# Optimization experiments

Hardware: AMD Instinct MI355X
Metric: run time of the kernel (lower is better)

The kernel has to match this reference:

```python
import jax, jax.numpy as jnp
import numpy as np

TOKENS = 8192
HIDDEN = 4096
EPS = 1e-6
FP8_MAX = 448.0  # max finite value of float8_e4m3fn


def setup_inputs() -> dict:
    key = jax.random.key(0)
    k1, k2, k3 = jax.random.split(key, 3)
    x = jax.random.normal(k1, (TOKENS, HIDDEN), jnp.float32)
    # RMSNorm gains near 1
    norm_w = 1.0 + 0.1 * jax.random.normal(k2, (4, HIDDEN), jnp.float32)
    Ws = 0.02 * jax.random.normal(k3, (3, HIDDEN, HIDDEN), jnp.float32)
    # static per-tensor weight scales (amax / fp8_max)
    w_scales = jnp.max(jnp.abs(Ws), axis=(1, 2)) / FP8_MAX
    return {"x": x, "norm_w": norm_w, "Ws": Ws, "w_scales": w_scales}


def _rmsnorm(x, w):
    var = jnp.mean(x * x, axis=-1, keepdims=True)
    return x * jax.lax.rsqrt(var + EPS) * w


def _quant_dequant_fp8(v, s):
    # quantize to e4m3 with scale s, then dequantize (emulated fp8 GEMM inputs)
    q = (v / s).astype(jnp.float8_e4m3fn)
    return q.astype(jnp.float32) * s


def _fp8_linear(y, W, w_scale):
    # dynamic per-token activation scale
    a_scale = jnp.maximum(jnp.max(jnp.abs(y), axis=-1, keepdims=True) / FP8_MAX, 1e-12)
    yq = _quant_dequant_fp8(y, a_scale)           # [T, H]
    Wq = _quant_dequant_fp8(W, w_scale)           # [H, H]
    return yq @ Wq.T                              # torch.nn.Linear convention


def reference(x, norm_w, Ws, w_scales):
    x = jax.nn.relu(x)
    resid = x
    y = _rmsnorm(x, norm_w[0])                    # plain RMSNorm
    for i in range(3):
        h = _fp8_linear(y, Ws[i], w_scales[i])    # FP8 GEMM
        resid = h + resid                         # fused add + RMSNorm
        y = _rmsnorm(resid, norm_w[i + 1])
    return y
```

## Files before the change

kernel.cpp:

```cpp
#include <hip/hip_runtime.h>
#include <stdint.h>

#define TOKENS 8192
#define HIDDEN 4096
constexpr float EPS = 1e-6f;
constexpr float FP8_MAX = 448.0f;

using f32x4  = __attribute__((ext_vector_type(4))) float;
using f32x16 = __attribute__((ext_vector_type(16))) float;
using i32x4  = __attribute__((ext_vector_type(4))) int;
using i32x8  = __attribute__((ext_vector_type(8))) int;

typedef __attribute__((address_space(3))) uint32_t lds_u32_t;
typedef const __attribute__((address_space(1))) uint32_t glb_u32_t;

__device__ inline uint32_t pack_fp8x4(float a, float b, float c, float d) {
    int w = 0;
    w = __builtin_amdgcn_cvt_pk_fp8_f32(a, b, w, false);
    w = __builtin_amdgcn_cvt_pk_fp8_f32(c, d, w, true);
    return (uint32_t)w;
}

__device__ inline float block_sum(float v, float* sh, int tid) {
#pragma unroll
    for (int o = 32; o > 0; o >>= 1) v += __shfl_xor(v, o, 64);
    if ((tid & 63) == 0) sh[tid >> 6] = v;
    __syncthreads();
    return sh[0] + sh[1] + sh[2] + sh[3];
}
__device__ inline float block_max(float v, float* sh, int tid) {
#pragma unroll
    for (int o = 32; o > 0; o >>= 1) v = fmaxf(v, __shfl_xor(v, o, 64));
    if ((tid & 63) == 0) sh[tid >> 6] = v;
    __syncthreads();
    return fmaxf(fmaxf(sh[0], sh[1]), fmaxf(sh[2], sh[3]));
}

__launch_bounds__(256)
__global__ void quant_weights(const float* __restrict__ Ws,
                              const float* __restrict__ w_scales,
                              uint8_t* __restrict__ Wq) {
    size_t idx = ((size_t)blockIdx.x * 256 + threadIdx.x) * 8;
    int tensor = (int)(idx / ((size_t)HIDDEN * HIDDEN));
    float inv = 1.0f / w_scales[tensor];
    const float4* src = (const float4*)(Ws + idx);
    float4 v0 = src[0], v1 = src[1];
    uint2 out;
    out.x = pack_fp8x4(v0.x * inv, v0.y * inv, v0.z * inv, v0.w * inv);
    out.y = pack_fp8x4(v1.x * inv, v1.y * inv, v1.z * inv, v1.w * inv);
    *(uint2*)(Wq + idx) = out;
}

__launch_bounds__(256)
__global__ void relu_rms_quant(const float* __restrict__ x,
                               const float* __restrict__ nw,
                               float* __restrict__ resid,
                               uint8_t* __restrict__ yq,
                               float* __restrict__ ascale) {
    __shared__ float sh1[4], sh2[4];
    const int row = blockIdx.x, tid = threadIdx.x;
    const float* xr = x + (size_t)row * HIDDEN;
    float* rr = resid + (size_t)row * HIDDEN;

    float4 v[4];
    float ss = 0.f;
#pragma unroll
    for (int c = 0; c < 4; ++c) {
        float4 t = *(const float4*)(xr + c * 1024 + tid * 4);
        t.x = fmaxf(t.x, 0.f); t.y = fmaxf(t.y, 0.f);
        t.z = fmaxf(t.z, 0.f); t.w = fmaxf(t.w, 0.f);
        v[c] = t;
        ss += t.x * t.x + t.y * t.y + t.z * t.z + t.w * t.w;
        *(float4*)(rr + c * 1024 + tid * 4) = t;
    }
    ss = block_sum(ss, sh1, tid);
    float rstd = 1.0f / sqrtf(ss * (1.0f / HIDDEN) + EPS);

    float4 y[4];
    float amax = 0.f;
#pragma unroll
    for (int c = 0; c < 4; ++c) {
        float4 w = *(const float4*)(nw + c * 1024 + tid * 4);
        y[c].x = v[c].x * rstd * w.x; amax = fmaxf(amax, fabsf(y[c].x));
        y[c].y = v[c].y * rstd * w.y; amax = fmaxf(amax, fabsf(y[c].y));
        y[c].z = v[c].z * rstd * w.z; amax = fmaxf(amax, fabsf(y[c].z));
        y[c].w = v[c].w * rstd * w.w; amax = fmaxf(amax, fabsf(y[c].w));
    }
    amax = block_max(amax, sh2, tid);
    float s = fmaxf(amax / FP8_MAX, 1e-12f);
    if (tid == 0) ascale[row] = s;
    float inv = 1.0f / s;
#pragma unroll
    for (int c = 0; c < 4; ++c) {
        uint32_t p = pack_fp8x4(y[c].x * inv, y[c].y * inv, y[c].z * inv, y[c].w * inv);
        *(uint32_t*)(yq + (size_t)row * HIDDEN + c * 1024 + tid * 4) = p;
    }
}

__launch_bounds__(256)
__global__ void rms_quant(const float* __restrict__ resid,
                          const float* __restrict__ nw,
                          uint8_t* __restrict__ yq,
                          float* __restrict__ ascale) {
    __shared__ float sh1[4], sh2[4];
    const int row = blockIdx.x, tid = threadIdx.x;
    const float* rr = resid + (size_t)row * HIDDEN;

    float4 v[4];
    float ss = 0.f;
#pragma unroll
    for (int c = 0; c < 4; ++c) {
        float4 t = *(const float4*)(rr + c * 1024 + tid * 4);
        v[c] = t;
        ss += t.x * t.x + t.y * t.y + t.z * t.z + t.w * t.w;
    }
    ss = block_sum(ss, sh1, tid);
    float rstd = 1.0f / sqrtf(ss * (1.0f / HIDDEN) + EPS);

    float4 y[4];
    float amax = 0.f;
#pragma unroll
    for (int c = 0; c < 4; ++c) {
        float4 w = *(const float4*)(nw + c * 1024 + tid * 4);
        y[c].x = v[c].x * rstd * w.x; amax = fmaxf(amax, fabsf(y[c].x));
        y[c].y = v[c].y * rstd * w.y; amax = fmaxf(amax, fabsf(y[c].y));
        y[c].z = v[c].z * rstd * w.z; amax = fmaxf(amax, fabsf(y[c].z));
        y[c].w = v[c].w * rstd * w.w; amax = fmaxf(amax, fabsf(y[c].w));
    }
    amax = block_max(amax, sh2, tid);
    float s = fmaxf(amax / FP8_MAX, 1e-12f);
    if (tid == 0) ascale[row] = s;
    float inv = 1.0f / s;
#pragma unroll
    for (int c = 0; c < 4; ++c) {
        uint32_t p = pack_fp8x4(y[c].x * inv, y[c].y * inv, y[c].z * inv, y[c].w * inv);
        *(uint32_t*)(yq + (size_t)row * HIDDEN + c * 1024 + tid * 4) = p;
    }
}

__launch_bounds__(256)
__global__ void rms_final(const float* __restrict__ resid,
                          const float* __restrict__ nw,
                          float* __restrict__ out) {
    __shared__ float sh1[4];
    const int row = blockIdx.x, tid = threadIdx.x;
    const float* rr = resid + (size_t)row * HIDDEN;

    float4 v[4];
    float ss = 0.f;
#pragma unroll
    for (int c = 0; c < 4; ++c) {
        float4 t = *(const float4*)(rr + c * 1024 + tid * 4);
        v[c] = t;
        ss += t.x * t.x + t.y * t.y + t.z * t.z + t.w * t.w;
    }
    ss = block_sum(ss, sh1, tid);
    float rstd = 1.0f / sqrtf(ss * (1.0f / HIDDEN) + EPS);

#pragma unroll
    for (int c = 0; c < 4; ++c) {
        float4 w = *(const float4*)(nw + c * 1024 + tid * 4);
        float4 o;
        o.x = v[c].x * rstd * w.x;
        o.y = v[c].y * rstd * w.y;
        o.z = v[c].z * rstd * w.z;
        o.w = v[c].w * rstd * w.w;
        *(float4*)(out + (size_t)row * HIDDEN + c * 1024 + tid * 4) = o;
    }
}

#define BM 128
#define BN 128
#define BK 64

__launch_bounds__(256)
__global__ void gemm_fp8(const uint8_t* __restrict__ Aq,
                         const uint8_t* __restrict__ Bq,
                         const float* __restrict__ ascale,
                         const float* __restrict__ wscale_p,
                         float* __restrict__ resid) {
    __shared__ __align__(16) uint8_t sA[2][BM * BK];
    __shared__ __align__(16) uint8_t sB[2][BN * BK];
    __shared__ float s_as[BM];

    const int tid = threadIdx.x;
    int bid = blockIdx.x;
    bid = (bid & 7) * 256 + (bid >> 3);
    const int nbn = HIDDEN / BN;
    const int bm = bid / nbn, bn = bid % nbn;
    const int brow = bm * BM, bcol = bn * BN;

    const int wave = tid >> 6, lane = tid & 63;
    const int wm = wave >> 1, wn = wave & 1;
    const int lr = lane & 31;
    const int lh = lane >> 5;

    if (tid < BM) s_as[tid] = ascale[brow + tid];

    f32x16 acc[2][2] = {};

    const uint8_t* aSrc = Aq + (size_t)brow * HIDDEN;
    const uint8_t* bSrc = Bq + (size_t)bcol * HIDDEN;

    const int r_st = tid >> 2;
    const int g_st = tid & 3;
    const int gsrc = g_st ^ ((r_st >> 1) & 3);
    const size_t off0 = (size_t)r_st * HIDDEN + gsrc * 16;
    const size_t off1 = (size_t)(r_st + 64) * HIDDEN + gsrc * 16;
    const int lds0 = wave * 1024;
    const int lds1 = 4096 + wave * 1024;

    int offA[2][2], offB[2][2];
#pragma unroll
    for (int m = 0; m < 2; ++m) {
        int ra = wm * 64 + m * 32 + lr;
        int sa_ = (ra >> 1) & 3;
        offA[m][0] = ra * 64 + ((2 * lh + 0) ^ sa_) * 16;
        offA[m][1] = ra * 64 + ((2 * lh + 1) ^ sa_) * 16;
        int rb = wn * 64 + m * 32 + lr;
        int sb_ = (rb >> 1) & 3;
        offB[m][0] = rb * 64 + ((2 * lh + 0) ^ sb_) * 16;
        offB[m][1] = rb * 64 + ((2 * lh + 1) ^ sb_) * 16;
    }

    const int UNIT = 0x7F7F7F7F;

    auto stage = [&](int buf, int k0) {
        __builtin_amdgcn_global_load_lds((glb_u32_t*)(aSrc + off0 + k0),
                                         (lds_u32_t*)&sA[buf][lds0], 16, 0, 0);
        __builtin_amdgcn_global_load_lds((glb_u32_t*)(aSrc + off1 + k0),
                                         (lds_u32_t*)&sA[buf][lds1], 16, 0, 0);
        __builtin_amdgcn_global_load_lds((glb_u32_t*)(bSrc + off0 + k0),
                                         (lds_u32_t*)&sB[buf][lds0], 16, 0, 0);
        __builtin_amdgcn_global_load_lds((glb_u32_t*)(bSrc + off1 + k0),
                                         (lds_u32_t*)&sB[buf][lds1], 16, 0, 0);
    };
    auto compute = [&](int buf) {
        i32x8 a[2], b[2];
#pragma unroll
        for (int m = 0; m < 2; ++m) {
            i32x4 lo = *(const i32x4*)&sA[buf][offA[m][0]];
            i32x4 hi = *(const i32x4*)&sA[buf][offA[m][1]];
            a[m] = __builtin_shufflevector(lo, hi, 0, 1, 2, 3, 4, 5, 6, 7);
        }
#pragma unroll
        for (int n = 0; n < 2; ++n) {
            i32x4 lo = *(const i32x4*)&sB[buf][offB[n][0]];
            i32x4 hi = *(const i32x4*)&sB[buf][offB[n][1]];
            b[n] = __builtin_shufflevector(lo, hi, 0, 1, 2, 3, 4, 5, 6, 7);
        }
#pragma unroll
        for (int m = 0; m < 2; ++m)
#pragma unroll
            for (int n = 0; n < 2; ++n)
                acc[m][n] = __builtin_amdgcn_mfma_scale_f32_32x32x64_f8f6f4(
                    a[m], b[n], acc[m][n], 0, 0, 0, UNIT, 0, UNIT);
    };

    stage(0, 0);
    __syncthreads();

    const int NT = HIDDEN / BK;
    for (int t = 0; t < NT; t += 2) {
        stage(1, (t + 1) * BK);
        compute(0);
        __syncthreads();
        if (t + 2 < NT) stage(0, (t + 2) * BK);
        compute(1);
        __syncthreads();
    }

    const float wsc = *wscale_p;
#pragma unroll
    for (int m = 0; m < 2; ++m)
#pragma unroll
        for (int n = 0; n < 2; ++n) {
            const int col = bcol + wn * 64 + n * 32 + lr;
#pragma unroll
            for (int i = 0; i < 16; ++i) {
                const int rl = (i & 3) + 8 * (i >> 2) + 4 * lh;
                const int row_local = wm * 64 + m * 32 + rl;
                const float alpha = s_as[row_local] * wsc;
                const size_t o = (size_t)(brow + row_local) * HIDDEN + col;
                resid[o] += acc[m][n][i] * alpha;
            }
        }
}

extern "C" void kernel_launch(void* const* d_in, const int* in_sizes, int n_in,
                              void* d_out, int out_size, void* d_ws, size_t ws_size,
                              hipStream_t stream) {
    const float* x   = (const float*)d_in[0];
    const float* nw  = (const float*)d_in[1];
    const float* Ws  = (const float*)d_in[2];
    const float* wsc = (const float*)d_in[3];
    float* out = (float*)d_out;

    uint8_t* ws = (uint8_t*)d_ws;
    float*   resid  = (float*)ws;
    uint8_t* yq     = ws + (size_t)TOKENS * HIDDEN * 4;
    uint8_t* Wq     = yq + (size_t)TOKENS * HIDDEN;
    float*   ascale = (float*)(Wq + (size_t)3 * HIDDEN * HIDDEN);

    quant_weights<<<(3 * (size_t)HIDDEN * HIDDEN) / 2048, 256, 0, stream>>>(Ws, wsc, Wq);

    relu_rms_quant<<<TOKENS, 256, 0, stream>>>(x, nw, resid, yq, ascale);

    for (int i = 0; i < 3; ++i) {
        gemm_fp8<<<(TOKENS / BM) * (HIDDEN / BN), 256, 0, stream>>>(
            yq, Wq + (size_t)i * HIDDEN * HIDDEN, ascale, wsc + i, resid);
        if (i < 2)
            rms_quant<<<TOKENS, 256, 0, stream>>>(resid, nw + (size_t)(i + 1) * HIDDEN, yq, ascale);
        else
            rms_final<<<TOKENS, 256, 0, stream>>>(resid, nw + (size_t)3 * HIDDEN, out);
    }
}
```

Measured before the change: 788.6 us.

## Enlarge FP8 GEMM tile to 256x256 with 4-stage LDS pipeline

The GEMM tile grows from 128x128 to 256x256 with 512 threads (8 waves, each owning a 128x64 sub-tile). Double buffering with two full barriers per k-step becomes a 4-buffer ring that prefetches two stages ahead, using explicit vmcnt waits and one barrier per step. MFMA issue is wrapped in s_setprio, and the per-row activation-scale load is moved after the main loop. The aim is more operand reuse per byte of global traffic and better hiding of load latency. The cost is 128 KB of LDS per block and higher register pressure, which may limit occupancy.

Result: faster. 691.0 us (-12.4%).

```diff
diff --git a/kernel.cpp b/kernel.cpp
--- a/kernel.cpp
+++ b/kernel.cpp
@@ -169,35 +169,34 @@
     }
 }
 
-#define BM 128
-#define BN 128
+#define BM 256
+#define BN 256
 #define BK 64
-
-__launch_bounds__(256)
+#define NBUF 4
+
+__launch_bounds__(512, 2)
 __global__ void gemm_fp8(const uint8_t* __restrict__ Aq,
                          const uint8_t* __restrict__ Bq,
                          const float* __restrict__ ascale,
                          const float* __restrict__ wscale_p,
                          float* __restrict__ resid) {
-    __shared__ __align__(16) uint8_t sA[2][BM * BK];
-    __shared__ __align__(16) uint8_t sB[2][BN * BK];
+    __shared__ __align__(16) uint8_t sA[NBUF][BM * BK];
+    __shared__ __align__(16) uint8_t sB[NBUF][BN * BK];
     __shared__ float s_as[BM];
 
     const int tid = threadIdx.x;
     int bid = blockIdx.x;
-    bid = (bid & 7) * 256 + (bid >> 3);
+    bid = (bid & 7) * 64 + (bid >> 3);
     const int nbn = HIDDEN / BN;
     const int bm = bid / nbn, bn = bid % nbn;
     const int brow = bm * BM, bcol = bn * BN;
 
     const int wave = tid >> 6, lane = tid & 63;
-    const int wm = wave >> 1, wn = wave & 1;
+    const int wm = wave >> 2, wn = wave & 3;
     const int lr = lane & 31;
     const int lh = lane >> 5;
 
-    if (tid < BM) s_as[tid] = ascale[brow + tid];
-
-    f32x16 acc[2][2] = {};
+    f32x16 acc[4][2] = {};
 
     const uint8_t* aSrc = Aq + (size_t)brow * HIDDEN;
     const uint8_t* bSrc = Bq + (size_t)bcol * HIDDEN;
@@ -206,83 +205,94 @@
     const int g_st = tid & 3;
     const int gsrc = g_st ^ ((r_st >> 1) & 3);
     const size_t off0 = (size_t)r_st * HIDDEN + gsrc * 16;
-    const size_t off1 = (size_t)(r_st + 64) * HIDDEN + gsrc * 16;
-    const int lds0 = wave * 1024;
-    const int lds1 = 4096 + wave * 1024;
-
-    int offA[2][2], offB[2][2];
-#pragma unroll
-    for (int m = 0; m < 2; ++m) {
-        int ra = wm * 64 + m * 32 + lr;
-        int sa_ = (ra >> 1) & 3;
-        offA[m][0] = ra * 64 + ((2 * lh + 0) ^ sa_) * 16;
-        offA[m][1] = ra * 64 + ((2 * lh + 1) ^ sa_) * 16;
-        int rb = wn * 64 + m * 32 + lr;
-        int sb_ = (rb >> 1) & 3;
-        offB[m][0] = rb * 64 + ((2 * lh + 0) ^ sb_) * 16;
-        offB[m][1] = rb * 64 + ((2 * lh + 1) ^ sb_) * 16;
+    const size_t off1 = (size_t)(r_st + 128) * HIDDEN + gsrc * 16;
+    const int ldsw = wave * 1024;
+
+    int offA[4][2], offB[2][2];
+#pragma unroll
+    for (int mi = 0; mi < 4; ++mi) {
+        int ra = wm * 128 + mi * 32 + lr;
+        int sw = (ra >> 1) & 3;
+        offA[mi][0] = ra * 64 + ((2 * lh + 0) ^ sw) * 16;
+        offA[mi][1] = ra * 64 + ((2 * lh + 1) ^ sw) * 16;
+    }
+#pragma unroll
+    for (int ni = 0; ni < 2; ++ni) {
+        int rb = wn * 64 + ni * 32 + lr;
+        int sw = (rb >> 1) & 3;
+        offB[ni][0] = rb * 64 + ((2 * lh + 0) ^ sw) * 16;
+        offB[ni][1] = rb * 64 + ((2 * lh + 1) ^ sw) * 16;
     }
 
     const int UNIT = 0x7F7F7F7F;
 
-    auto stage = [&](int buf, int k0) {
+    auto stage = [&](int buf, int kt) {
+        const int k0 = kt * BK;
         __builtin_amdgcn_global_load_lds((glb_u32_t*)(aSrc + off0 + k0),
-                                         (lds_u32_t*)&sA[buf][lds0], 16, 0, 0);
+                                         (lds_u32_t*)&sA[buf][ldsw], 16, 0, 0);
         __builtin_amdgcn_global_load_lds((glb_u32_t*)(aSrc + off1 + k0),
-                                         (lds_u32_t*)&sA[buf][lds1], 16, 0, 0);
+                                         (lds_u32_t*)&sA[buf][8192 + ldsw], 16, 0, 0);
         __builtin_amdgcn_global_load_lds((glb_u32_t*)(bSrc + off0 + k0),
-                                         (lds_u32_t*)&sB[buf][lds0], 16, 0, 0);
+                                         (lds_u32_t*)&sB[buf][ldsw], 16, 0, 0);
         __builtin_amdgcn_global_load_lds((glb_u32_t*)(bSrc + off1 + k0),
-                                         (lds_u32_t*)&sB[buf][lds1], 16, 0, 0);
+                                         (lds_u32_t*)&sB[buf][8192 + ldsw], 16, 0, 0);
     };
     auto compute = [&](int buf) {
-        i32x8 a[2], b[2];
-#pragma unroll
-        for (int m = 0; m < 2; ++m) {
-            i32x4 lo = *(const i32x4*)&sA[buf][offA[m][0]];
-            i32x4 hi = *(const i32x4*)&sA[buf][offA[m][1]];
-            a[m] = __builtin_shufflevector(lo, hi, 0, 1, 2, 3, 4, 5, 6, 7);
+        i32x8 a[4], b[2];
+#pragma unroll
+        for (int mi = 0; mi < 4; ++mi) {
+            i32x4 lo = *(const i32x4*)&sA[buf][offA[mi][0]];
+            i32x4 hi = *(const i32x4*)&sA[buf][offA[mi][1]];
+            a[mi] = __builtin_shufflevector(lo, hi, 0, 1, 2, 3, 4, 5, 6, 7);
         }
 #pragma unroll
-        for (int n = 0; n < 2; ++n) {
-            i32x4 lo = *(const i32x4*)&sB[buf][offB[n][0]];
-            i32x4 hi = *(const i32x4*)&sB[buf][offB[n][1]];
-            b[n] = __builtin_shufflevector(lo, hi, 0, 1, 2, 3, 4, 5, 6, 7);
+        for (int ni = 0; ni < 2; ++ni) {
+            i32x4 lo = *(const i32x4*)&sB[buf][offB[ni][0]];
+            i32x4 hi = *(const i32x4*)&sB[buf][offB[ni][1]];
+            b[ni] = __builtin_shufflevector(lo, hi, 0, 1, 2, 3, 4, 5, 6, 7);
         }
-#pragma unroll
-        for (int m = 0; m < 2; ++m)
-#pragma unroll
-            for (int n = 0; n < 2; ++n)
-                acc[m][n] = __builtin_amdgcn_mfma_scale_f32_32x32x64_f8f6f4(
-                    a[m], b[n], acc[m][n], 0, 0, 0, UNIT, 0, UNIT);
+        __builtin_amdgcn_s_setprio(1);
+#pragma unroll
+        for (int mi = 0; mi < 4; ++mi)
+#pragma unroll
+            for (int ni = 0; ni < 2; ++ni)
+                acc[mi][ni] = __builtin_amdgcn_mfma_scale_f32_32x32x64_f8f6f4(
+                    a[mi], b[ni], acc[mi][ni], 0, 0, 0, UNIT, 0, UNIT);
+        __builtin_amdgcn_s_setprio(0);
     };
 
+    const int NT = HIDDEN / BK;
     stage(0, 0);
+    stage(1, 1);
+    for (int t = 0; t < NT; ++t) {
+        if (t + 2 < NT) {
+            stage((t + 2) & 3, t + 2);
+            asm volatile("s_waitcnt vmcnt(8)" ::: "memory");
+        } else if (t + 1 < NT) {
+            asm volatile("s_waitcnt vmcnt(4)" ::: "memory");
+        } else {
+            asm volatile("s_waitcnt vmcnt(0)" ::: "memory");
+        }
+        __builtin_amdgcn_s_barrier();
+        compute(t & 3);
+    }
+
+    if (tid < BM) s_as[tid] = ascale[brow + tid];
     __syncthreads();
 
-    const int NT = HIDDEN / BK;
-    for (int t = 0; t < NT; t += 2) {
-        stage(1, (t + 1) * BK);
-        compute(0);
-        __syncthreads();
-        if (t + 2 < NT) stage(0, (t + 2) * BK);
-        compute(1);
-        __syncthreads();
-    }
-
     const float wsc = *wscale_p;
 #pragma unroll
-    for (int m = 0; m < 2; ++m)
-#pragma unroll
-        for (int n = 0; n < 2; ++n) {
-            const int col = bcol + wn * 64 + n * 32 + lr;
+    for (int mi = 0; mi < 4; ++mi)
+#pragma unroll
+        for (int ni = 0; ni < 2; ++ni) {
+            const int col = bcol + wn * 64 + ni * 32 + lr;
 #pragma unroll
             for (int i = 0; i < 16; ++i) {
                 const int rl = (i & 3) + 8 * (i >> 2) + 4 * lh;
-                const int row_local = wm * 64 + m * 32 + rl;
+                const int row_local = wm * 128 + mi * 32 + rl;
                 const float alpha = s_as[row_local] * wsc;
                 const size_t o = (size_t)(brow + row_local) * HIDDEN + col;
-                resid[o] += acc[m][n][i] * alpha;
+                resid[o] += acc[mi][ni][i] * alpha;
             }
         }
 }
@@ -307,7 +317,7 @@
     relu_rms_quant<<<TOKENS, 256, 0, stream>>>(x, nw, resid, yq, ascale);
 
     for (int i = 0; i < 3; ++i) {
-        gemm_fp8<<<(TOKENS / BM) * (HIDDEN / BN), 256, 0, stream>>>(
+        gemm_fp8<<<(TOKENS / BM) * (HIDDEN / BN), 512, 0, stream>>>(
             yq, Wq + (size_t)i * HIDDEN * HIDDEN, ascale, wsc + i, resid);
         if (i < 2)
             rms_quant<<<TOKENS, 256, 0, stream>>>(resid, nw + (size_t)(i + 1) * HIDDEN, yq, ascale);
```
